# Kernel tuning notes

Measured on AMD Instinct MI355X. Metric: run time of the kernel, lower is better.

The kernel has to match this reference:

```python
import jax, jax.numpy as jnp
import numpy as np

B, S, H = 2, 1024, 4544
NH, HD = 71, 64          # 71 query heads, head_dim 64, 1 shared kv head (multi-query)
THETA = 10000.0
NEG_INF = -1e9


def setup_inputs() -> dict:
    key = jax.random.key(0)
    k1, k2, k3 = jax.random.split(key, 3)
    hidden_states = jax.random.normal(k1, (B, S, H), dtype=jnp.float32)
    W_qkv = jax.random.normal(k2, (H, H + 2 * HD), dtype=jnp.float32) * 0.02
    W_dense = jax.random.normal(k3, (H, H), dtype=jnp.float32) * 0.02
    causal = jnp.tril(jnp.ones((S, S), dtype=bool))
    attention_mask = jnp.where(causal, 0.0, NEG_INF).astype(jnp.float32)[None, None]  # [1,1,S,S]
    position_ids = jnp.arange(S, dtype=jnp.int32)[None]  # [1,S]
    return {"hidden_states": hidden_states, "W_qkv": W_qkv, "W_dense": W_dense,
            "attention_mask": attention_mask, "position_ids": position_ids}


def _rope_cos_sin(position_ids):
    # HF FalconRotaryEmbedding: inv_freq over even dims, emb = cat(freqs, freqs)
    inv_freq = 1.0 / (THETA ** (jnp.arange(0, HD, 2, dtype=jnp.float32) / HD))
    freqs = position_ids.astype(jnp.float32)[..., None] * inv_freq  # [1,S,HD/2]
    emb = jnp.concatenate([freqs, freqs], axis=-1)                  # [1,S,HD]
    return jnp.cos(emb)[:, None], jnp.sin(emb)[:, None]             # [1,1,S,HD]


def _rotate_half(x):
    return jnp.concatenate([-x[..., HD // 2:], x[..., :HD // 2]], axis=-1)


def reference(hidden_states, W_qkv, W_dense, attention_mask, position_ids):
    # fused QKV projection (bias=False for Falcon-7B)
    fused = hidden_states @ W_qkv                       # [B,S,(NH+2)*HD]
    fused = fused.reshape(B, S, NH + 2, HD)
    q = jnp.transpose(fused[:, :, :NH], (0, 2, 1, 3))          # [B,NH,S,HD]
    k = jnp.transpose(fused[:, :, NH:NH + 1], (0, 2, 1, 3))    # [B,1,S,HD]
    v = jnp.transpose(fused[:, :, NH + 1:], (0, 2, 1, 3))      # [B,1,S,HD]

    cos, sin = _rope_cos_sin(position_ids)
    q = q * cos + _rotate_half(q) * sin
    k = k * cos + _rotate_half(k) * sin

    # scores: shared kv head broadcasts across the 71 query heads
    scores = jnp.matmul(q, jnp.swapaxes(k, -1, -2)) * (1.0 / np.sqrt(HD))  # [B,NH,S,S]
    probs = jax.nn.softmax(scores + attention_mask, axis=-1)
    attn = jnp.matmul(probs, v)                                            # [B,NH,S,HD]

    attn = jnp.transpose(attn, (0, 2, 1, 3)).reshape(B, S, NH * HD)
    return attn @ W_dense
```

## Files before the change

### kernel.cpp

```cpp
#include <hip/hip_runtime.h>

typedef unsigned short u16;
using f32x4  = __attribute__((ext_vector_type(4))) float;
using f32x16 = __attribute__((ext_vector_type(16))) float;
using s16x8  = __attribute__((ext_vector_type(8))) short;

static __device__ __forceinline__ u16 f2b(float f) {
  unsigned int u = __builtin_bit_cast(unsigned int, f);
  u = (u + 0x7fffu + ((u >> 16) & 1u)) >> 16;
  return (u16)u;
}
static __device__ __forceinline__ float b2f(u16 h) {
  unsigned int u = ((unsigned int)h) << 16;
  return __builtin_bit_cast(float, u);
}
static __device__ __forceinline__ unsigned int cvtpk(float lo, float hi) {
  unsigned int r;
  asm("v_cvt_pk_bf16_f32 %0, %1, %2" : "=v"(r) : "v"(lo), "v"(hi));
  return r;
}
static __device__ __forceinline__ void gload16(const void* g, void* l) {
  __builtin_amdgcn_global_load_lds(
      (const __attribute__((address_space(1))) void*)g,
      (__attribute__((address_space(3))) void*)l, 16, 0, 0);
}

__global__ __launch_bounds__(256) void conv_bf16(
    const float* __restrict__ in, u16* __restrict__ out, int n8)
{
  int i = blockIdx.x * 256 + threadIdx.x;
  if (i >= n8) return;
  float4 a = *(const float4*)(in + (size_t)i * 8);
  float4 b = *(const float4*)(in + (size_t)i * 8 + 4);
  __align__(16) u16 tmp[8] = {f2b(a.x), f2b(a.y), f2b(a.z), f2b(a.w),
                              f2b(b.x), f2b(b.y), f2b(b.z), f2b(b.w)};
  *(uint4*)(out + (size_t)i * 8) = *(const uint4*)tmp;
}

__global__ __launch_bounds__(256) void transpose_conv(
    const float* __restrict__ W, u16* __restrict__ Wt, int K, int N)
{
  __shared__ u16 tile[64][72];
  const int t = threadIdx.x;
  const int n0 = blockIdx.x * 64, k0 = blockIdx.y * 64;
  #pragma unroll
  for (int i = 0; i < 4; ++i) {
    int idx = i * 256 + t;
    int r = idx >> 4;
    int c = (idx & 15) << 2;
    float4 v = make_float4(0.f, 0.f, 0.f, 0.f);
    if (n0 + c < N) v = *(const float4*)(W + (size_t)(k0 + r) * N + n0 + c);
    tile[r][c + 0] = f2b(v.x);
    tile[r][c + 1] = f2b(v.y);
    tile[r][c + 2] = f2b(v.z);
    tile[r][c + 3] = f2b(v.w);
  }
  __syncthreads();
  #pragma unroll
  for (int i = 0; i < 2; ++i) {
    int idx = i * 256 + t;
    int rn = idx >> 3;
    int c8 = (idx & 7) << 3;
    __align__(16) u16 tmp[8];
    #pragma unroll
    for (int j = 0; j < 8; ++j) tmp[j] = tile[c8 + j][rn];
    *(uint4*)(Wt + (size_t)(n0 + rn) * K + k0 + c8) = *(const uint4*)tmp;
  }
}

template<int MODE>
__global__ __launch_bounds__(256) void gemm_bt(
    const u16* __restrict__ A, const u16* __restrict__ B,
    float* __restrict__ Cptr,
    u16* __restrict__ qo, u16* __restrict__ ko, u16* __restrict__ vo,
    const int* __restrict__ pos,
    int M, int N, int K, int NBX)
{
  __shared__ __align__(16) u16 aLds[128 * 32];
  __shared__ __align__(16) u16 bLds[128 * 32];

  const int t = threadIdx.x, lane = t & 63, w = t >> 6;
  const int lr = lane & 15, lg = lane >> 4;
  const int wr = w >> 1, wc = w & 1;

  const int bid = blockIdx.x;
  const int qq  = gridDim.x >> 3;
  const int swz = (bid & 7) * qq + (bid >> 3);
  const int m0 = (swz / NBX) * 128, n0 = (swz % NBX) * 128;

  const int srow = lane >> 2;
  const int skc  = (lane & 3) << 3;

  f32x4 acc[4][4] = {};

  const int nk = K >> 5;
  for (int kt = 0; kt < nk; ++kt) {
    const int k0 = kt << 5;
    __syncthreads();
    #pragma unroll
    for (int i = 0; i < 2; ++i) {
      int row = i * 64 + w * 16 + srow;
      gload16(A + (size_t)(m0 + row) * K + k0 + skc,
              (char*)aLds + i * 4096 + w * 1024);
      gload16(B + (size_t)(n0 + row) * K + k0 + skc,
              (char*)bLds + i * 4096 + w * 1024);
    }
    __syncthreads();
    s16x8 af[4], bf[4];
    #pragma unroll
    for (int m = 0; m < 4; ++m)
      af[m] = *(const s16x8*)(aLds + (wr * 64 + m * 16 + lr) * 32 + lg * 8);
    #pragma unroll
    for (int n = 0; n < 4; ++n)
      bf[n] = *(const s16x8*)(bLds + (wc * 64 + n * 16 + lr) * 32 + lg * 8);
    #pragma unroll
    for (int m = 0; m < 4; ++m)
      #pragma unroll
      for (int n = 0; n < 4; ++n)
        acc[m][n] = __builtin_amdgcn_mfma_f32_16x16x32_bf16(af[m], bf[n], acc[m][n], 0, 0, 0);
  }

  if constexpr (MODE == 0) {
    #pragma unroll
    for (int m = 0; m < 4; ++m) {
      int row = m0 + wr * 64 + m * 16 + lg * 4;
      #pragma unroll
      for (int n = 0; n < 4; ++n) {
        int col = n0 + wc * 64 + n * 16 + lr;
        if (col < N) {
          #pragma unroll
          for (int r = 0; r < 4; ++r)
            Cptr[(size_t)(row + r) * N + col] = acc[m][n][r];
        }
      }
    }
  } else {
    const int h = (n0 + wc * 64) >> 6;
    if (h > 72) return;
    const float inv0 = exp2f(-0.41524101186092029f * (float)lr);
    const float inv1 = exp2f(-0.41524101186092029f * (float)(16 + lr));
    #pragma unroll
    for (int m = 0; m < 4; ++m) {
      #pragma unroll
      for (int r = 0; r < 4; ++r) {
        int row = m0 + wr * 64 + m * 16 + lg * 4 + r;
        int b = row >> 10, s = row & 1023;
        if (h == 72) {
          #pragma unroll
          for (int n = 0; n < 4; ++n) {
            int d = n * 16 + lr;
            vo[((size_t)b * 64 + d) * 1024 + s] = f2b(acc[m][n][r]);
          }
        } else {
          float p = (float)pos[s];
          float sn0, cs0, sn1, cs1;
          __sincosf(p * inv0, &sn0, &cs0);
          __sincosf(p * inv1, &sn1, &cs1);
          #pragma unroll
          for (int n = 0; n < 4; ++n) {
            float cs  = (n & 1) ? cs1 : cs0;
            float sn  = (n & 1) ? sn1 : sn0;
            float sgn = (n < 2) ? -1.f : 1.f;
            float val = acc[m][n][r] * cs + sgn * acc[m][n ^ 2][r] * sn;
            int d = n * 16 + lr;
            if (h < 71)
              qo[((size_t)(b * 71 + h) * 1024 + s) * 64 + d] = f2b(val);
            else
              ko[((size_t)b * 1024 + s) * 64 + d] = f2b(val);
          }
        }
      }
    }
  }
}

__global__ __launch_bounds__(128) void attn_kernel(
    const u16* __restrict__ q, const u16* __restrict__ kx,
    const u16* __restrict__ vT, u16* __restrict__ attnO)
{
  const int t = threadIdx.x, lane = t & 63, w = t >> 6;
  const int lq  = lane & 31;
  const int hi  = lane >> 5;
  const int hi4 = hi << 2;
  const int pair = blockIdx.x, h = blockIdx.y, b = blockIdx.z;
  const int qt = w ? (31 - pair) : pair;
  const int q0 = qt * 32;

  const u16* qbase = q + ((size_t)(b * 71 + h) * 1024 + q0 + lq) * 64 + hi * 8;
  s16x8 qf[4];
  #pragma unroll
  for (int kt = 0; kt < 4; ++kt) qf[kt] = *(const s16x8*)(qbase + kt * 16);

  f32x16 o0 = {}, o1 = {};
  float m = -1e30f, l = 0.f;

  const u16* kbase  = kx + ((size_t)b * 1024 + lq) * 64 + hi * 8;
  const u16* vbase0 = vT + ((size_t)b * 64 + lq) * 1024 + hi * 8;
  const u16* vbase1 = vbase0 + 32 * 1024;

  for (int it = 0; it <= qt; ++it) {
    const int kv0 = it * 32;
    s16x8 kf[4];
    #pragma unroll
    for (int kt = 0; kt < 4; ++kt)
      kf[kt] = *(const s16x8*)(kbase + (size_t)kv0 * 64 + kt * 16);
    s16x8 v00 = *(const s16x8*)(vbase0 + kv0);
    s16x8 v01 = *(const s16x8*)(vbase0 + kv0 + 16);
    s16x8 v10 = *(const s16x8*)(vbase1 + kv0);
    s16x8 v11 = *(const s16x8*)(vbase1 + kv0 + 16);

    f32x16 sa = {}, sb = {};
    sa = __builtin_amdgcn_mfma_f32_32x32x16_bf16(kf[0], qf[0], sa, 0, 0, 0);
    sb = __builtin_amdgcn_mfma_f32_32x32x16_bf16(kf[1], qf[1], sb, 0, 0, 0);
    sa = __builtin_amdgcn_mfma_f32_32x32x16_bf16(kf[2], qf[2], sa, 0, 0, 0);
    sb = __builtin_amdgcn_mfma_f32_32x32x16_bf16(kf[3], qf[3], sb, 0, 0, 0);

    float s[16];
    float pmax = -1e30f;
    if (it == qt) {
      #pragma unroll
      for (int r = 0; r < 16; ++r) {
        int R = (r & 3) + ((r >> 2) << 3) + hi4;
        s[r] = (R > lq) ? -1e30f : (sa[r] + sb[r]) * 0.125f;
        pmax = fmaxf(pmax, s[r]);
      }
    } else {
      #pragma unroll
      for (int r = 0; r < 16; ++r) {
        s[r] = (sa[r] + sb[r]) * 0.125f;
        pmax = fmaxf(pmax, s[r]);
      }
    }
    pmax = fmaxf(pmax, __shfl_xor(pmax, 32));

    if (!__all(pmax <= m + 8.f)) {
      float mn = fmaxf(m, pmax);
      float corr = __expf(m - mn);
      m = mn;
      l *= corr;
      #pragma unroll
      for (int r = 0; r < 16; ++r) {
        float c2 = __shfl(corr, (r & 3) + ((r >> 2) << 3) + hi4);
        o0[r] *= c2; o1[r] *= c2;
      }
    }

    float p[16], sum = 0.f;
    #pragma unroll
    for (int r = 0; r < 16; ++r) { p[r] = __expf(s[r] - m); sum += p[r]; }
    sum += __shfl_xor(sum, 32);
    l += sum;

    unsigned int a0 = cvtpk(p[0], p[1]),   a1 = cvtpk(p[2], p[3]);
    unsigned int b0 = cvtpk(p[4], p[5]),   b1 = cvtpk(p[6], p[7]);
    asm("v_permlane32_swap_b32 %0, %1" : "+v"(a0), "+v"(b0));
    asm("v_permlane32_swap_b32 %0, %1" : "+v"(a1), "+v"(b1));
    unsigned int c0 = cvtpk(p[8], p[9]),   c1 = cvtpk(p[10], p[11]);
    unsigned int d0 = cvtpk(p[12], p[13]), d1 = cvtpk(p[14], p[15]);
    asm("v_permlane32_swap_b32 %0, %1" : "+v"(c0), "+v"(d0));
    asm("v_permlane32_swap_b32 %0, %1" : "+v"(c1), "+v"(d1));
    union { unsigned int wd[4]; s16x8 v; } palo, pahi;
    palo.wd[0] = a0; palo.wd[1] = a1; palo.wd[2] = b0; palo.wd[3] = b1;
    pahi.wd[0] = c0; pahi.wd[1] = c1; pahi.wd[2] = d0; pahi.wd[3] = d1;

    o0 = __builtin_amdgcn_mfma_f32_32x32x16_bf16(palo.v, v00, o0, 0, 0, 0);
    o0 = __builtin_amdgcn_mfma_f32_32x32x16_bf16(pahi.v, v01, o0, 0, 0, 0);
    o1 = __builtin_amdgcn_mfma_f32_32x32x16_bf16(palo.v, v10, o1, 0, 0, 0);
    o1 = __builtin_amdgcn_mfma_f32_32x32x16_bf16(pahi.v, v11, o1, 0, 0, 0);
  }

  float linv = 1.f / l;
  #pragma unroll
  for (int r = 0; r < 16; ++r) {
    int R = (r & 3) + ((r >> 2) << 3) + hi4;
    float c2 = __shfl(linv, R);
    size_t base = ((size_t)(b * 1024 + q0 + R) * 71 + h) * 64;
    attnO[base + lq]      = f2b(o0[r] * c2);
    attnO[base + 32 + lq] = f2b(o1[r] * c2);
  }
}

extern "C" void kernel_launch(void* const* d_in, const int* in_sizes, int n_in,
                              void* d_out, int out_size, void* d_ws, size_t ws_size,
                              hipStream_t stream) {
  const float* hidden = (const float*)d_in[0];
  const float* Wqkv   = (const float*)d_in[1];
  const float* Wdense = (const float*)d_in[2];
  const int*   pos    = (const int*)d_in[4];
  float* out = (float*)d_out;

  char* wsp = (char*)d_ws;
  u16* Wt    = (u16*)(wsp);
  u16* A1    = (u16*)(wsp + 43040768);
  u16* qws   = (u16*)(wsp + 43040768 + 18612224);
  u16* kws   = (u16*)(wsp + 43040768 + 18612224 + 18612224);
  u16* vws   = (u16*)(wsp + 43040768 + 18612224 + 18612224 + 262144);
  u16* attnw = A1;

  conv_bf16<<<4544, 256, 0, stream>>>(hidden, A1, 2048 * 4544 / 8);
  transpose_conv<<<dim3(74, 71), 256, 0, stream>>>(Wqkv, Wt, 4544, 4672);
  gemm_bt<2><<<592, 256, 0, stream>>>(A1, Wt, nullptr, qws, kws, vws, pos,
                                      2048, 4672, 4544, 37);
  transpose_conv<<<dim3(72, 71), 256, 0, stream>>>(Wdense, Wt, 4544, 4544);
  attn_kernel<<<dim3(16, 71, 2), 128, 0, stream>>>(qws, kws, vws, attnw);
  gemm_bt<0><<<576, 256, 0, stream>>>(attnw, Wt, out, nullptr, nullptr, nullptr,
                                      nullptr, 2048, 4544, 4544, 36);
}
```

Before: 448.7 us.

## Double-buffer GEMM LDS tiles with BK=64 and XOR-swizzled layout

```diff
diff --git a/kernel.cpp b/kernel.cpp
--- a/kernel.cpp
+++ b/kernel.cpp
@@ -76,8 +76,8 @@
     const int* __restrict__ pos,
     int M, int N, int K, int NBX)
 {
-  __shared__ __align__(16) u16 aLds[128 * 32];
-  __shared__ __align__(16) u16 bLds[128 * 32];
+  __shared__ __align__(16) u16 aLds[2][128 * 64];
+  __shared__ __align__(16) u16 bLds[2][128 * 64];
 
   const int t = threadIdx.x, lane = t & 63, w = t >> 6;
   const int lr = lane & 15, lg = lane >> 4;
@@ -88,37 +88,56 @@
   const int swz = (bid & 7) * qq + (bid >> 3);
   const int m0 = (swz / NBX) * 128, n0 = (swz % NBX) * 128;
 
-  const int srow = lane >> 2;
-  const int skc  = (lane & 3) << 3;
+  const int srow = lane >> 3;
+  const int ssw  = ((lane & 7) ^ srow) << 3;
 
   f32x4 acc[4][4] = {};
-
-  const int nk = K >> 5;
+  const int nk = K >> 6;
+
+#define STAGE(buf, tt) do {                                                   \
+    size_t kq_ = (size_t)(tt) << 6;                                           \
+    _Pragma("unroll")                                                         \
+    for (int u_ = 0; u_ < 4; ++u_) {                                          \
+      int row_ = u_ * 32 + w * 8 + srow;                                      \
+      gload16(A + (size_t)(m0 + row_) * K + kq_ + ssw,                        \
+              (char*)&aLds[buf][0] + u_ * 4096 + w * 1024);                   \
+      gload16(B + (size_t)(n0 + row_) * K + kq_ + ssw,                        \
+              (char*)&bLds[buf][0] + u_ * 4096 + w * 1024);                   \
+    }                                                                         \
+  } while (0)
+
+  STAGE(0, 0);
   for (int kt = 0; kt < nk; ++kt) {
-    const int k0 = kt << 5;
-    __syncthreads();
-    #pragma unroll
-    for (int i = 0; i < 2; ++i) {
-      int row = i * 64 + w * 16 + srow;
-      gload16(A + (size_t)(m0 + row) * K + k0 + skc,
-              (char*)aLds + i * 4096 + w * 1024);
-      gload16(B + (size_t)(n0 + row) * K + k0 + skc,
-              (char*)bLds + i * 4096 + w * 1024);
-    }
-    __syncthreads();
+    const int cur = kt & 1;
+    if (kt + 1 < nk) {
+      STAGE(cur ^ 1, kt + 1);
+      asm volatile("s_waitcnt vmcnt(8)" ::: "memory");
+    } else {
+      asm volatile("s_waitcnt vmcnt(0)" ::: "memory");
+    }
+    __builtin_amdgcn_s_barrier();
+    __builtin_amdgcn_sched_barrier(0);
+    const char* ab = (const char*)&aLds[cur][0];
+    const char* bb = (const char*)&bLds[cur][0];
     s16x8 af[4], bf[4];
     #pragma unroll
-    for (int m = 0; m < 4; ++m)
-      af[m] = *(const s16x8*)(aLds + (wr * 64 + m * 16 + lr) * 32 + lg * 8);
-    #pragma unroll
-    for (int n = 0; n < 4; ++n)
-      bf[n] = *(const s16x8*)(bLds + (wc * 64 + n * 16 + lr) * 32 + lg * 8);
-    #pragma unroll
-    for (int m = 0; m < 4; ++m)
+    for (int kk = 0; kk < 2; ++kk) {
+      const int csw = ((kk << 6) | (lg << 4)) ^ ((lr & 7) << 4);
+      #pragma unroll
+      for (int m = 0; m < 4; ++m)
+        af[m] = *(const s16x8*)(ab + (wr * 64 + m * 16 + lr) * 128 + csw);
       #pragma unroll
       for (int n = 0; n < 4; ++n)
-        acc[m][n] = __builtin_amdgcn_mfma_f32_16x16x32_bf16(af[m], bf[n], acc[m][n], 0, 0, 0);
-  }
+        bf[n] = *(const s16x8*)(bb + (wc * 64 + n * 16 + lr) * 128 + csw);
+      #pragma unroll
+      for (int m = 0; m < 4; ++m)
+        #pragma unroll
+        for (int n = 0; n < 4; ++n)
+          acc[m][n] = __builtin_amdgcn_mfma_f32_16x16x32_bf16(af[m], bf[n], acc[m][n], 0, 0, 0);
+    }
+    __builtin_amdgcn_s_barrier();
+  }
+#undef STAGE
 
   if constexpr (MODE == 0) {
     #pragma unroll
```

Measured after the change: 451.7 us. Within noise of the previous version (+0.7%).
